# Kernel optimization log

Measured on AMD Instinct MI355X. Metric: run time of the kernel, lower is better.

Reference implementation:

```python
import jax, jax.numpy as jnp
import numpy as np

B, N, C, H, T = 64, 4096, 768, 12, 10


def setup_inputs() -> dict:
    key = jax.random.key(0)
    kx, kq, kk, kv, kp = jax.random.split(key, 5)
    std = 0.02  # trunc_normal std from _init_weights
    return {
        "x": jax.random.normal(kx, (B, N, C), jnp.float32),
        "Wq": std * jax.random.normal(kq, (C, C), jnp.float32),
        "Wk": std * jax.random.normal(kk, (C, C), jnp.float32),
        "Wv": std * jax.random.normal(kv, (C, C), jnp.float32),
        "Wp": std * jax.random.normal(kp, (C, C), jnp.float32),
        "bp": jnp.zeros((C,), jnp.float32),
        "nb_task_tokens": T,
    }


def reference(x, Wq, Wk, Wv, Wp, bp, nb_task_tokens):
    Bq, Nq, Cq = x.shape
    d = Cq // H
    scale = d ** -0.5
    Tt = nb_task_tokens
    # q only from the first T (task) tokens; k, v from all N tokens
    q = (x[:, :Tt] @ Wq).reshape(Bq, Tt, H, d).transpose(0, 2, 1, 3) * scale  # [B,H,T,d]
    k = (x @ Wk).reshape(Bq, Nq, H, d).transpose(0, 2, 1, 3)                  # [B,H,N,d]
    v = (x @ Wv).reshape(Bq, Nq, H, d).transpose(0, 2, 1, 3)                  # [B,H,N,d]
    attn = jnp.einsum("bhtd,bhnd->bhtn", q, k)                                # [B,H,T,N]
    # mask: task token i may attend to itself and to all patch tokens (cols >= T),
    # but not to other task tokens
    rows = jnp.arange(Tt)[:, None]
    cols = jnp.arange(Nq)[None, :]
    allowed = (cols >= Tt) | (cols == rows)                                   # [T,N]
    attn = jnp.where(allowed, attn, -jnp.inf)
    attn = jax.nn.softmax(attn, axis=-1)
    x_cls = jnp.einsum("bhtn,bhnd->bhtd", attn, v)                            # [B,H,T,d]
    x_cls = x_cls.transpose(0, 2, 1, 3).reshape(Bq, Tt, Cq)
    x_cls = x_cls @ Wp + bp
    return (x_cls, attn, v)
```

## Files before the change

kernel.cpp:

```cpp
#include <hip/hip_runtime.h>

typedef __attribute__((ext_vector_type(8))) short short8;
typedef __attribute__((ext_vector_type(4))) short short4v;
typedef __attribute__((ext_vector_type(4))) float f32x4;

__device__ __forceinline__ unsigned short f2bf(float f) {
  union { float f; unsigned u; } v; v.f = f;
  unsigned r = v.u + 0x7FFFu + ((v.u >> 16) & 1u);
  return (unsigned short)(r >> 16);
}

__device__ __forceinline__ float bf2f(unsigned short h) {
  union { unsigned u; float f; } v; v.u = ((unsigned)h) << 16;
  return v.f;
}

__device__ __forceinline__ void gload16(const void* g, void* l) {
  __builtin_amdgcn_global_load_lds(
      (const __attribute__((address_space(1))) void*)g,
      (__attribute__((address_space(3))) void*)l, 16, 0, 0);
}

__global__ __launch_bounds__(256) void conv_x(const float* __restrict__ x,
                                              unsigned short* __restrict__ xb) {
  const long total = 25165824;
  long stride = (long)gridDim.x * 256;
  for (long u = blockIdx.x * 256 + threadIdx.x; u < total; u += stride) {
    const float* p = x + u * 8;
    float4 a = *(const float4*)p;
    float4 b = *(const float4*)(p + 4);
    short8 h;
    h[0] = (short)f2bf(a.x); h[1] = (short)f2bf(a.y);
    h[2] = (short)f2bf(a.z); h[3] = (short)f2bf(a.w);
    h[4] = (short)f2bf(b.x); h[5] = (short)f2bf(b.y);
    h[6] = (short)f2bf(b.z); h[7] = (short)f2bf(b.w);
    *(short8*)(xb + u * 8) = h;
  }
}

__global__ __launch_bounds__(256) void prep_w(const float* __restrict__ Wk,
                                              const float* __restrict__ Wv,
                                              unsigned short* __restrict__ Wt) {
  int idx = blockIdx.x * 256 + threadIdx.x;
  int n = idx / 768, k = idx - n * 768;
  float w = (n < 768) ? Wk[k * 768 + n] : Wv[k * 768 + (n - 768)];
  Wt[idx] = f2bf(w);
}

__global__ __launch_bounds__(256) void q_proj(const float* __restrict__ x,
                                              const float* __restrict__ Wq,
                                              unsigned short* __restrict__ q_ws) {
  int b = blockIdx.x, tid = threadIdx.x;
  __shared__ float xr[7680];
  const float* xp = x + (long)b * 4096 * 768;
  for (int i = tid; i < 7680; i += 256) xr[i] = xp[i];
  for (int i = tid; i < 12 * 6 * 64; i += 256) {
    int h = i / 384, rem = i - h * 384;
    int t = 10 + rem / 64, d = rem & 63;
    q_ws[(((long)(b * 12 + h) * 16 + t) << 6) + d] = 0;
  }
  __syncthreads();
  float acc[10][3];
#pragma unroll
  for (int t = 0; t < 10; ++t) { acc[t][0] = 0.f; acc[t][1] = 0.f; acc[t][2] = 0.f; }
  for (int k = 0; k < 768; ++k) {
    const float* wr = Wq + (long)k * 768;
    float w0 = wr[tid], w1 = wr[tid + 256], w2 = wr[tid + 512];
#pragma unroll
    for (int t = 0; t < 10; ++t) {
      float xv = xr[t * 768 + k];
      acc[t][0] += xv * w0; acc[t][1] += xv * w1; acc[t][2] += xv * w2;
    }
  }
#pragma unroll
  for (int t = 0; t < 10; ++t) {
#pragma unroll
    for (int j = 0; j < 3; ++j) {
      int c = tid + j * 256;
      int h = c >> 6, d = c & 63;
      q_ws[(((long)(b * 12 + h) * 16 + t) << 6) + d] = f2bf(acc[t][j] * 0.125f);
    }
  }
}

#define SGA(AT, I, KO) gload16(sA + (long)(I) * 49152 + (KO), (AT) + ((I) * 64 + uw * 8) * 64)
#define SGB(BT, I, KO) gload16(sB + (long)(I) * 49152 + (KO), (BT) + ((I) * 64 + uw * 8) * 64)
#define WBND asm volatile("s_waitcnt vmcnt(0)\n\ts_barrier" ::: "memory")
#define PBAR __builtin_amdgcn_s_barrier()

#define BODY(AC, BC, AN, BN, KOS, DOST)                                         \
  {                                                                             \
    short8 fa[4][2], fb0[2][2], fb1[2][2];                                      \
    if (DOST) { SGA(AN, 0, KOS); SGA(AN, 1, KOS); SGB(BN, 0, KOS); SGB(BN, 1, KOS); } \
    _Pragma("unroll")                                                           \
    for (int mi = 0; mi < 4; ++mi) {                                            \
      fa[mi][0] = *(const short8*)&AC[arb + mi * 1024 + ck0];                   \
      fa[mi][1] = *(const short8*)&AC[arb + mi * 1024 + ck1];                   \
    }                                                                           \
    _Pragma("unroll")                                                           \
    for (int ni = 0; ni < 2; ++ni) {                                            \
      fb0[ni][0] = *(const short8*)&BC[brb + ni * 1024 + ck0];                  \
      fb0[ni][1] = *(const short8*)&BC[brb + ni * 1024 + ck1];                  \
    }                                                                           \
    PBAR;                                                                       \
    __builtin_amdgcn_s_setprio(1);                                              \
    _Pragma("unroll")                                                           \
    for (int mi = 0; mi < 4; ++mi)                                              \
      _Pragma("unroll")                                                         \
      for (int ni = 0; ni < 2; ++ni) {                                          \
        acc[mi][ni] = __builtin_amdgcn_mfma_f32_16x16x32_bf16(fa[mi][0], fb0[ni][0], acc[mi][ni], 0, 0, 0); \
        acc[mi][ni] = __builtin_amdgcn_mfma_f32_16x16x32_bf16(fa[mi][1], fb0[ni][1], acc[mi][ni], 0, 0, 0); \
      }                                                                         \
    __builtin_amdgcn_s_setprio(0);                                              \
    PBAR;                                                                       \
    if (DOST) { SGA(AN, 2, KOS); SGA(AN, 3, KOS); SGB(BN, 2, KOS); SGB(BN, 3, KOS); } \
    _Pragma("unroll")                                                           \
    for (int ni = 0; ni < 2; ++ni) {                                            \
      fb1[ni][0] = *(const short8*)&BC[brb + (ni + 2) * 1024 + ck0];            \
      fb1[ni][1] = *(const short8*)&BC[brb + (ni + 2) * 1024 + ck1];            \
    }                                                                           \
    PBAR;                                                                       \
    __builtin_amdgcn_s_setprio(1);                                              \
    _Pragma("unroll")                                                           \
    for (int mi = 0; mi < 4; ++mi)                                              \
      _Pragma("unroll")                                                         \
      for (int ni = 0; ni < 2; ++ni) {                                          \
        acc[mi][ni + 2] = __builtin_amdgcn_mfma_f32_16x16x32_bf16(fa[mi][0], fb1[ni][0], acc[mi][ni + 2], 0, 0, 0); \
        acc[mi][ni + 2] = __builtin_amdgcn_mfma_f32_16x16x32_bf16(fa[mi][1], fb1[ni][1], acc[mi][ni + 2], 0, 0, 0); \
      }                                                                         \
    __builtin_amdgcn_s_setprio(0);                                              \
    PBAR;                                                                       \
    _Pragma("unroll")                                                           \
    for (int mi = 0; mi < 4; ++mi) {                                            \
      fa[mi][0] = *(const short8*)&AC[arb + (mi + 4) * 1024 + ck0];             \
      fa[mi][1] = *(const short8*)&AC[arb + (mi + 4) * 1024 + ck1];             \
    }                                                                           \
    PBAR;                                                                       \
    __builtin_amdgcn_s_setprio(1);                                              \
    _Pragma("unroll")                                                           \
    for (int mi = 0; mi < 4; ++mi)                                              \
      _Pragma("unroll")                                                         \
      for (int ni = 0; ni < 2; ++ni) {                                          \
        acc[mi + 4][ni + 2] = __builtin_amdgcn_mfma_f32_16x16x32_bf16(fa[mi][0], fb1[ni][0], acc[mi + 4][ni + 2], 0, 0, 0); \
        acc[mi + 4][ni + 2] = __builtin_amdgcn_mfma_f32_16x16x32_bf16(fa[mi][1], fb1[ni][1], acc[mi + 4][ni + 2], 0, 0, 0); \
      }                                                                         \
    __builtin_amdgcn_s_setprio(0);                                              \
    PBAR;                                                                       \
    __builtin_amdgcn_s_setprio(1);                                              \
    _Pragma("unroll")                                                           \
    for (int mi = 0; mi < 4; ++mi)                                              \
      _Pragma("unroll")                                                         \
      for (int ni = 0; ni < 2; ++ni) {                                          \
        acc[mi + 4][ni] = __builtin_amdgcn_mfma_f32_16x16x32_bf16(fa[mi][0], fb0[ni][0], acc[mi + 4][ni], 0, 0, 0); \
        acc[mi + 4][ni] = __builtin_amdgcn_mfma_f32_16x16x32_bf16(fa[mi][1], fb0[ni][1], acc[mi + 4][ni], 0, 0, 0); \
      }                                                                         \
    __builtin_amdgcn_s_setprio(0);                                              \
  }

#define GEMM_PROLOGUE                                                           \
  int bid = blockIdx.x;                                                         \
  int lb = (bid & 7) * 768 + (bid >> 3);                                        \
  int mt = lb / 6;                                                              \
  int nt = lb - mt * 6;                                                         \
  long m0 = (long)mt * 256;                                                     \
  int n0 = nt * 256;                                                            \
  int tid = threadIdx.x;                                                        \
  int lane = tid & 63;                                                          \
  int uw = __builtin_amdgcn_readfirstlane(tid >> 6);                            \
  int wm = uw >> 2;                                                             \
  int wn = uw & 3;                                                              \
  int r16 = lane & 15;                                                          \
  int gk = lane >> 4;                                                           \
  const unsigned short* xs = xb + m0 * 768;                                     \
  const unsigned short* wp = Wt + (long)n0 * 768;                               \
  int srow8 = lane >> 3;                                                        \
  int sch = ((lane & 7) ^ (srow8 & 7)) << 3;                                    \
  const unsigned short* sA = xs + (long)(uw * 8 + srow8) * 768 + sch;           \
  const unsigned short* sB = wp + (long)(uw * 8 + srow8) * 768 + sch;           \
  int ck0 = ((gk ^ (r16 & 7)) << 3);                                            \
  int ck1 = (((4 + gk) ^ (r16 & 7)) << 3);                                      \
  int arb = (wm * 128 + r16) * 64;                                              \
  int brb = (wn * 64 + r16) * 64;                                               \
  f32x4 acc[8][4];                                                              \
  _Pragma("unroll")                                                             \
  for (int i = 0; i < 8; ++i)                                                   \
    _Pragma("unroll")                                                           \
    for (int j = 0; j < 4; ++j) acc[i][j] = (f32x4){0.f, 0.f, 0.f, 0.f};        \
  SGA(A0T, 0, 0); SGA(A0T, 1, 0); SGA(A0T, 2, 0); SGA(A0T, 3, 0);               \
  SGB(B0T, 0, 0); SGB(B0T, 1, 0); SGB(B0T, 2, 0); SGB(B0T, 3, 0);               \
  WBND;                                                                         \
  _Pragma("unroll 1")                                                           \
  for (int t = 0; t < 12; t += 2) {                                             \
    BODY(A0T, B0T, A1T, B1T, (t + 1) * 64, true);                               \
    WBND;                                                                       \
    BODY(A1T, B1T, A0T, B0T, (t + 2) * 64, (t + 2) < 12);                       \
    WBND;                                                                       \
  }

__global__ __launch_bounds__(512, 2) void gemm_kv9(const unsigned short* __restrict__ xb,
                                                   const unsigned short* __restrict__ Wt,
                                                   unsigned short* __restrict__ k_ws,
                                                   float* __restrict__ v_out,
                                                   unsigned short* __restrict__ vt) {
  __shared__ char smem[131072];
  unsigned short* A0T = (unsigned short*)(smem);
  unsigned short* B0T = (unsigned short*)(smem + 32768);
  unsigned short* A1T = (unsigned short*)(smem + 65536);
  unsigned short* B1T = (unsigned short*)(smem + 98304);
  GEMM_PROLOGUE

  float* scr0 = (float*)smem + uw * 2176;
  float* scr1 = scr0 + 1088;
  bool is_k = (n0 < 768);
  int h = (is_k ? (n0 >> 6) : ((n0 - 768) >> 6)) + wn;
  int bq = (int)(m0 >> 12);
  int nb = (int)(m0 & 4095) + wm * 128;

  if (is_k) {
#pragma unroll
    for (int mi = 0; mi < 8; ++mi) {
#pragma unroll
      for (int ni = 0; ni < 4; ++ni)
#pragma unroll
        for (int r = 0; r < 4; ++r)
          scr0[(gk * 4 + r) * 68 + ni * 16 + r16] = acc[mi][ni][r];
      int nbase = nb + mi * 16;
#pragma unroll
      for (int p = 0; p < 2; ++p) {
        int row = p * 8 + (lane >> 3);
        int d0 = (lane & 7) << 3;
        float4 aa = *(const float4*)&scr0[row * 68 + d0];
        float4 bb = *(const float4*)&scr0[row * 68 + d0 + 4];
        short8 hh;
        hh[0] = (short)f2bf(aa.x); hh[1] = (short)f2bf(aa.y);
        hh[2] = (short)f2bf(aa.z); hh[3] = (short)f2bf(aa.w);
        hh[4] = (short)f2bf(bb.x); hh[5] = (short)f2bf(bb.y);
        hh[6] = (short)f2bf(bb.z); hh[7] = (short)f2bf(bb.w);
        *(short8*)&k_ws[((long)(bq * 12 + h) * 4096 + nbase + row) * 64 + d0] = hh;
      }
    }
  } else {
    unsigned short* vTp = vt + ((long)(bq * 12 + h) * 64) * 4096;
#pragma unroll
    for (int mp = 0; mp < 4; ++mp) {
      int nbase = nb + mp * 32;
#pragma unroll
      for (int ni = 0; ni < 4; ++ni)
#pragma unroll
        for (int r = 0; r < 4; ++r) {
          scr0[(gk * 4 + r) * 68 + ni * 16 + r16] = acc[mp * 2][ni][r];
          scr1[(gk * 4 + r) * 68 + ni * 16 + r16] = acc[mp * 2 + 1][ni][r];
        }
#pragma unroll
      for (int p = 0; p < 4; ++p) {
        int row = p * 4 + (lane >> 4);
        int d0 = (lane & 15) << 2;
        float4 a0 = *(const float4*)&scr0[row * 68 + d0];
        *(float4*)&v_out[((long)(bq * 12 + h) * 4096 + nbase + row) * 64 + d0] = a0;
        float4 a1 = *(const float4*)&scr1[row * 68 + d0];
        *(float4*)&v_out[((long)(bq * 12 + h) * 4096 + nbase + 16 + row) * 64 + d0] = a1;
      }
      short8 w0;
      short8 w1;
      short8 w2;
      short8 w3;
#pragma unroll
      for (int i = 0; i < 8; ++i) {
        w0[i] = (short)f2bf(scr0[i * 68 + lane]);
        w1[i] = (short)f2bf(scr0[(i + 8) * 68 + lane]);
        w2[i] = (short)f2bf(scr1[i * 68 + lane]);
        w3[i] = (short)f2bf(scr1[(i + 8) * 68 + lane]);
      }
      unsigned short* vrow = vTp + (long)lane * 4096 + nbase;
      *(short8*)(vrow)      = w0;
      *(short8*)(vrow + 8)  = w1;
      *(short8*)(vrow + 16) = w2;
      *(short8*)(vrow + 24) = w3;
    }
  }
}

__global__ __launch_bounds__(512, 2) void gemm_kv8(const unsigned short* __restrict__ xb,
                                                   const unsigned short* __restrict__ Wt,
                                                   unsigned short* __restrict__ k_ws,
                                                   float* __restrict__ v_out) {
  __shared__ char smem[131072];
  unsigned short* A0T = (unsigned short*)(smem);
  unsigned short* B0T = (unsigned short*)(smem + 32768);
  unsigned short* A1T = (unsigned short*)(smem + 65536);
  unsigned short* B1T = (unsigned short*)(smem + 98304);
  GEMM_PROLOGUE

  float* scr = (float*)smem + uw * 1088;
  bool is_k = (n0 < 768);
  int h = (is_k ? (n0 >> 6) : ((n0 - 768) >> 6)) + wn;
  int bq = (int)(m0 >> 12);
  int nb = (int)(m0 & 4095) + wm * 128;
#pragma unroll
  for (int mi = 0; mi < 8; ++mi) {
#pragma unroll
    for (int ni = 0; ni < 4; ++ni)
#pragma unroll
      for (int r = 0; r < 4; ++r)
        scr[(gk * 4 + r) * 68 + ni * 16 + r16] = acc[mi][ni][r];
    int nbase = nb + mi * 16;
    if (is_k) {
#pragma unroll
      for (int p = 0; p < 2; ++p) {
        int row = p * 8 + (lane >> 3);
        int d0 = (lane & 7) << 3;
        float4 aa = *(const float4*)&scr[row * 68 + d0];
        float4 bb = *(const float4*)&scr[row * 68 + d0 + 4];
        short8 hh;
        hh[0] = (short)f2bf(aa.x); hh[1] = (short)f2bf(aa.y);
        hh[2] = (short)f2bf(aa.z); hh[3] = (short)f2bf(aa.w);
        hh[4] = (short)f2bf(bb.x); hh[5] = (short)f2bf(bb.y);
        hh[6] = (short)f2bf(bb.z); hh[7] = (short)f2bf(bb.w);
        *(short8*)&k_ws[((long)(bq * 12 + h) * 4096 + nbase + row) * 64 + d0] = hh;
      }
    } else {
#pragma unroll
      for (int p = 0; p < 4; ++p) {
        int row = p * 4 + (lane >> 4);
        int d0 = (lane & 15) << 2;
        float4 aa = *(const float4*)&scr[row * 68 + d0];
        *(float4*)&v_out[((long)(bq * 12 + h) * 4096 + nbase + row) * 64 + d0] = aa;
      }
    }
  }
}

#undef GEMM_PROLOGUE
#undef BODY
#undef SGA
#undef SGB
#undef WBND
#undef PBAR

__global__ __launch_bounds__(256) void gemm_kv(const float* __restrict__ x,
                                               const unsigned short* __restrict__ Wt,
                                               unsigned short* __restrict__ k_ws,
                                               float* __restrict__ v_out) {
  __shared__ char lds[32768];
  int bid = blockIdx.x;
  int lb = (bid & 7) * 3072 + (bid >> 3);
  int mt = lb / 12, nt = lb - mt * 12;
  long m0 = (long)mt * 128; int n0 = nt * 128;
  int tid = threadIdx.x, lane = tid & 63;
  int wid = tid >> 6, wm = wid >> 1, wn = wid & 1;
  int rlo = lane & 15, gk = lane >> 4;

  const float* xs = x + m0 * 768;
  const unsigned short* wp = Wt + (long)n0 * 768;

  int arow0 = tid >> 3, ak4 = (tid & 7) << 2;
  int bn = tid >> 1, bg = (tid & 1) << 1;

  f32x4 acc[4][4];
#pragma unroll
  for (int i = 0; i < 4; ++i)
#pragma unroll
    for (int j = 0; j < 4; ++j) acc[i][j] = (f32x4){0.f, 0.f, 0.f, 0.f};

  float4 fA[4]; short8 wB[2];
#pragma unroll
  for (int it = 0; it < 4; ++it) {
    int row = it * 32 + arow0;
    fA[it] = *(const float4*)(xs + (long)row * 768 + ak4);
  }
#pragma unroll
  for (int i = 0; i < 2; ++i)
    wB[i] = *(const short8*)(wp + (long)bn * 768 + (bg + i) * 8);
#pragma unroll
  for (int it = 0; it < 4; ++it) {
    int row = it * 32 + arow0;
    short4v h;
    h[0] = (short)f2bf(fA[it].x); h[1] = (short)f2bf(fA[it].y);
    h[2] = (short)f2bf(fA[it].z); h[3] = (short)f2bf(fA[it].w);
    *(short4v*)(lds + row * 64 + ((ak4 * 2) ^ (((row >> 1) & 3) << 4))) = h;
  }
#pragma unroll
  for (int i = 0; i < 2; ++i)
    *(short8*)(lds + 16384 + bn * 64 + (((bg + i) * 16) ^ (((bn >> 1) & 3) << 4))) = wB[i];
  __syncthreads();

#pragma unroll 2
  for (int ks = 0; ks < 24; ++ks) {
    char* Ab = lds + (ks & 1) * 8192;
    char* Bb = lds + 16384 + (ks & 1) * 8192;
    bool pf = (ks + 1 < 24);
    if (pf) {
#pragma unroll
      for (int it = 0; it < 4; ++it) {
        int row = it * 32 + arow0;
        fA[it] = *(const float4*)(xs + (long)row * 768 + (ks + 1) * 32 + ak4);
      }
#pragma unroll
      for (int i = 0; i < 2; ++i)
        wB[i] = *(const short8*)(wp + (long)bn * 768 + (ks + 1) * 32 + (bg + i) * 8);
    }
    short8 af[4], bfr[4];
#pragma unroll
    for (int mi = 0; mi < 4; ++mi) {
      int row = wm * 64 + mi * 16 + rlo;
      af[mi] = *(const short8*)(Ab + row * 64 + ((gk * 16) ^ (((row >> 1) & 3) << 4)));
    }
#pragma unroll
    for (int ni = 0; ni < 4; ++ni) {
      int n = wn * 64 + ni * 16 + rlo;
      bfr[ni] = *(const short8*)(Bb + n * 64 + ((gk * 16) ^ (((n >> 1) & 3) << 4)));
    }
#pragma unroll
    for (int mi = 0; mi < 4; ++mi)
#pragma unroll
      for (int ni = 0; ni < 4; ++ni)
        acc[mi][ni] = __builtin_amdgcn_mfma_f32_16x16x32_bf16(af[mi], bfr[ni], acc[mi][ni], 0, 0, 0);
    if (pf) {
      char* An = lds + ((ks + 1) & 1) * 8192;
      char* Bn = lds + 16384 + ((ks + 1) & 1) * 8192;
#pragma unroll
      for (int it = 0; it < 4; ++it) {
        int row = it * 32 + arow0;
        short4v h;
        h[0] = (short)f2bf(fA[it].x); h[1] = (short)f2bf(fA[it].y);
        h[2] = (short)f2bf(fA[it].z); h[3] = (short)f2bf(fA[it].w);
        *(short4v*)(An + row * 64 + ((ak4 * 2) ^ (((row >> 1) & 3) << 4))) = h;
      }
#pragma unroll
      for (int i = 0; i < 2; ++i)
        *(short8*)(Bn + bn * 64 + (((bg + i) * 16) ^ (((bn >> 1) & 3) << 4))) = wB[i];
    }
    __syncthreads();
  }

  bool is_k = (n0 < 768);
  int cb = is_k ? n0 : n0 - 768;
#pragma unroll
  for (int ni = 0; ni < 4; ++ni) {
    int cc = cb + wn * 64 + ni * 16 + rlo;
    int h = cc >> 6, d = cc & 63;
#pragma unroll
    for (int mi = 0; mi < 4; ++mi) {
#pragma unroll
      for (int r = 0; r < 4; ++r) {
        long m = m0 + wm * 64 + mi * 16 + gk * 4 + r;
        int b = (int)(m >> 12), n = (int)(m & 4095);
        long off = ((long)(b * 12 + h) * 4096 + n) * 64 + d;
        float val = acc[mi][ni][r];
        if (is_k) k_ws[off] = f2bf(val);
        else      v_out[off] = val;
      }
    }
  }
}

__global__ __launch_bounds__(512) void attn_fused4(const unsigned short* __restrict__ k_ws,
                                                   const unsigned short* __restrict__ q_ws,
                                                   const unsigned short* __restrict__ vt,
                                                   float* __restrict__ attn_out,
                                                   float* __restrict__ preproj) {
  __shared__ char blob[115712];
  unsigned short* pbuf = (unsigned short*)blob;
  float* part = (float*)(blob + 81920);
  float* redm = (float*)(blob + 114688);
  float* rowmax16 = redm + 128;
  float* rowinv16 = rowmax16 + 16;

  int tid = threadIdx.x, lane = tid & 63, w = tid >> 6;
  int bh = blockIdx.x;
  int r16 = lane & 15, gk = lane >> 4;
  int trc = (r16 < 10) ? r16 : 9;
  int nW = w << 9;

  const unsigned short* kp = k_ws + (long)bh * (4096 * 64);
  const unsigned short* qp = q_ws + (long)bh * 1024;
  float* sraw = attn_out + (long)bh * 40960;
  const unsigned short* vtp = vt + (long)bh * (64 * 4096);

  short8 qf0 = *(const short8*)(qp + r16 * 64 + gk * 8);
  short8 qf1 = *(const short8*)(qp + r16 * 64 + 32 + gk * 8);

  char* pbw = (char*)pbuf + w * 10240 + r16 * 1024;
  int swz = (r16 & 7) << 4;

  float pmax = -3.0e38f;
#pragma unroll 4
  for (int ch = 0; ch < 32; ++ch) {
    int n0 = nW + (ch << 4);
    short8 kf0 = *(const short8*)(kp + (long)(n0 + r16) * 64 + gk * 8);
    short8 kf1 = *(const short8*)(kp + (long)(n0 + r16) * 64 + 32 + gk * 8);
    f32x4 d4 = (f32x4){0.f, 0.f, 0.f, 0.f};
    d4 = __builtin_amdgcn_mfma_f32_16x16x32_bf16(kf0, qf0, d4, 0, 0, 0);
    d4 = __builtin_amdgcn_mfma_f32_16x16x32_bf16(kf1, qf1, d4, 0, 0, 0);
#pragma unroll
    for (int r = 0; r < 4; ++r) {
      int n = n0 + gk * 4 + r;
      float v = d4[r];
      if (n < 10 && n != r16) v = -1e30f;
      d4[r] = v;
      pmax = fmaxf(pmax, v);
    }
    if (r16 < 10) {
      short4v h4;
      h4[0] = (short)f2bf(d4[0]); h4[1] = (short)f2bf(d4[1]);
      h4[2] = (short)f2bf(d4[2]); h4[3] = (short)f2bf(d4[3]);
      *(short4v*)(pbw + ((ch * 32 + gk * 8) ^ swz)) = h4;
    }
  }
  pmax = fmaxf(pmax, __shfl_xor(pmax, 16));
  pmax = fmaxf(pmax, __shfl_xor(pmax, 32));
  if (lane < 16) redm[w * 16 + lane] = pmax;
  __syncthreads();
  if (tid < 16) {
    float m = redm[tid];
#pragma unroll
    for (int i = 1; i < 8; ++i) m = fmaxf(m, redm[i * 16 + tid]);
    rowmax16[tid] = m;
  }
  __syncthreads();

  float mx = rowmax16[trc];
  char* pbr = (char*)pbuf + w * 10240 + trc * 1024;
  int swr = (trc & 7) << 4;
  float psum = 0.f;
#pragma unroll 4
  for (int i = 0; i < 16; ++i) {
    short8 sv = *(const short8*)(pbr + ((i * 64 + gk * 16) ^ swr));
#pragma unroll
    for (int j = 0; j < 8; ++j) psum += __expf(bf2f((unsigned short)sv[j]) - mx);
  }
  psum += __shfl_xor(psum, 16);
  psum += __shfl_xor(psum, 32);
  if (lane < 16) redm[w * 16 + lane] = psum;
  __syncthreads();
  if (tid < 16) {
    float t = 0.f;
#pragma unroll
    for (int i = 0; i < 8; ++i) t += redm[i * 16 + tid];
    rowinv16[tid] = 1.0f / t;
  }
  __syncthreads();
  float inv = rowinv16[trc];

  if (r16 < 10) {
#pragma unroll 4
    for (int i = 0; i < 16; ++i) {
      short8 sv = *(const short8*)(pbw + ((i * 64 + gk * 16) ^ swz));
      float4 o0, o1;
      o0.x = __expf(bf2f((unsigned short)sv[0]) - mx) * inv;
      o0.y = __expf(bf2f((unsigned short)sv[1]) - mx) * inv;
      o0.z = __expf(bf2f((unsigned short)sv[2]) - mx) * inv;
      o0.w = __expf(bf2f((unsigned short)sv[3]) - mx) * inv;
      o1.x = __expf(bf2f((unsigned short)sv[4]) - mx) * inv;
      o1.y = __expf(bf2f((unsigned short)sv[5]) - mx) * inv;
      o1.z = __expf(bf2f((unsigned short)sv[6]) - mx) * inv;
      o1.w = __expf(bf2f((unsigned short)sv[7]) - mx) * inv;
      float* gp = sraw + r16 * 4096 + nW + i * 32 + gk * 8;
      *(float4*)gp = o0;
      *(float4*)(gp + 4) = o1;
    }
  }

  f32x4 pacc[4];
#pragma unroll
  for (int dc = 0; dc < 4; ++dc) pacc[dc] = (f32x4){0.f, 0.f, 0.f, 0.f};
#pragma unroll 2
  for (int ks = 0; ks < 16; ++ks) {
    short8 raw = *(const short8*)(pbr + ((ks * 64 + gk * 16) ^ swr));
    short8 pa;
#pragma unroll
    for (int j = 0; j < 8; ++j)
      pa[j] = (short)f2bf(__expf(bf2f((unsigned short)raw[j]) - mx) * inv);
    int nbb = nW + ks * 32 + gk * 8;
#pragma unroll
    for (int dc = 0; dc < 4; ++dc) {
      short8 vb = *(const short8*)&vtp[(long)(dc * 16 + r16) * 4096 + nbb];
      pacc[dc] = __builtin_amdgcn_mfma_f32_16x16x32_bf16(pa, vb, pacc[dc], 0, 0, 0);
    }
  }
#pragma unroll
  for (int dc = 0; dc < 4; ++dc)
#pragma unroll
    for (int r = 0; r < 4; ++r)
      part[w * 1024 + dc * 256 + (gk * 4 + r) * 16 + r16] = pacc[dc][r];
  __syncthreads();

  int b = bh / 12, h = bh - b * 12;
  for (int idx = tid; idx < 640; idx += 512) {
    int tt = idx >> 6, d = idx & 63;
    int dc = d >> 4, dl = d & 15;
    float sum = 0.f;
#pragma unroll
    for (int i = 0; i < 8; ++i) sum += part[i * 1024 + dc * 256 + tt * 16 + dl];
    preproj[((long)b * 10 + tt) * 768 + h * 64 + d] = sum;
  }
}

__global__ __launch_bounds__(512) void attn_fused3(const unsigned short* __restrict__ k_ws,
                                                   const unsigned short* __restrict__ q_ws,
                                                   const float* __restrict__ v_glob,
                                                   float* __restrict__ attn_out,
                                                   float* __restrict__ preproj) {
  __shared__ char blob[115712];
  unsigned short* pbuf = (unsigned short*)blob;
  float* part = (float*)(blob + 81920);
  float* redm = (float*)(blob + 114688);
  float* rowmax16 = redm + 128;
  float* rowinv16 = rowmax16 + 16;

  int tid = threadIdx.x, lane = tid & 63, w = tid >> 6;
  int bh = blockIdx.x;
  int r16 = lane & 15, gk = lane >> 4;
  int trc = (r16 < 10) ? r16 : 9;
  int nW = w << 9;

  const unsigned short* kp = k_ws + (long)bh * (4096 * 64);
  const unsigned short* qp = q_ws + (long)bh * 1024;
  float* sraw = attn_out + (long)bh * 40960;
  const float* vp = v_glob + (long)bh * (4096 * 64);

  short8 qf0 = *(const short8*)(qp + r16 * 64 + gk * 8);
  short8 qf1 = *(const short8*)(qp + r16 * 64 + 32 + gk * 8);

  char* pbw = (char*)pbuf + w * 10240 + r16 * 1024;
  int swz = (r16 & 7) << 4;

  float pmax = -3.0e38f;
#pragma unroll 4
  for (int ch = 0; ch < 32; ++ch) {
    int n0 = nW + (ch << 4);
    short8 kf0 = *(const short8*)(kp + (long)(n0 + r16) * 64 + gk * 8);
    short8 kf1 = *(const short8*)(kp + (long)(n0 + r16) * 64 + 32 + gk * 8);
    f32x4 d4 = (f32x4){0.f, 0.f, 0.f, 0.f};
    d4 = __builtin_amdgcn_mfma_f32_16x16x32_bf16(kf0, qf0, d4, 0, 0, 0);
    d4 = __builtin_amdgcn_mfma_f32_16x16x32_bf16(kf1, qf1, d4, 0, 0, 0);
#pragma unroll
    for (int r = 0; r < 4; ++r) {
      int n = n0 + gk * 4 + r;
      float v = d4[r];
      if (n < 10 && n != r16) v = -1e30f;
      d4[r] = v;
      pmax = fmaxf(pmax, v);
    }
    if (r16 < 10) {
      short4v h4;
      h4[0] = (short)f2bf(d4[0]); h4[1] = (short)f2bf(d4[1]);
      h4[2] = (short)f2bf(d4[2]); h4[3] = (short)f2bf(d4[3]);
      *(short4v*)(pbw + ((ch * 32 + gk * 8) ^ swz)) = h4;
    }
  }
  pmax = fmaxf(pmax, __shfl_xor(pmax, 16));
  pmax = fmaxf(pmax, __shfl_xor(pmax, 32));
  if (lane < 16) redm[w * 16 + lane] = pmax;
  __syncthreads();
  if (tid < 16) {
    float m = redm[tid];
#pragma unroll
    for (int i = 1; i < 8; ++i) m = fmaxf(m, redm[i * 16 + tid]);
    rowmax16[tid] = m;
  }
  __syncthreads();

  float mx = rowmax16[trc];
  char* pbr = (char*)pbuf + w * 10240 + trc * 1024;
  int swr = (trc & 7) << 4;
  float psum = 0.f;
#pragma unroll 4
  for (int i = 0; i < 16; ++i) {
    short8 sv = *(const short8*)(pbr + ((i * 64 + gk * 16) ^ swr));
#pragma unroll
    for (int j = 0; j < 8; ++j) psum += __expf(bf2f((unsigned short)sv[j]) - mx);
  }
  psum += __shfl_xor(psum, 16);
  psum += __shfl_xor(psum, 32);
  if (lane < 16) redm[w * 16 + lane] = psum;
  __syncthreads();
  if (tid < 16) {
    float t = 0.f;
#pragma unroll
    for (int i = 0; i < 8; ++i) t += redm[i * 16 + tid];
    rowinv16[tid] = 1.0f / t;
  }
  __syncthreads();
  float inv = rowinv16[trc];

  if (r16 < 10) {
#pragma unroll 4
    for (int i = 0; i < 16; ++i) {
      short8 sv = *(const short8*)(pbw + ((i * 64 + gk * 16) ^ swz));
      float4 o0, o1;
      o0.x = __expf(bf2f((unsigned short)sv[0]) - mx) * inv;
      o0.y = __expf(bf2f((unsigned short)sv[1]) - mx) * inv;
      o0.z = __expf(bf2f((unsigned short)sv[2]) - mx) * inv;
      o0.w = __expf(bf2f((unsigned short)sv[3]) - mx) * inv;
      o1.x = __expf(bf2f((unsigned short)sv[4]) - mx) * inv;
      o1.y = __expf(bf2f((unsigned short)sv[5]) - mx) * inv;
      o1.z = __expf(bf2f((unsigned short)sv[6]) - mx) * inv;
      o1.w = __expf(bf2f((unsigned short)sv[7]) - mx) * inv;
      float* gp = sraw + r16 * 4096 + nW + i * 32 + gk * 8;
      *(float4*)gp = o0;
      *(float4*)(gp + 4) = o1;
    }
  }

  f32x4 pacc[4];
#pragma unroll
  for (int dc = 0; dc < 4; ++dc) pacc[dc] = (f32x4){0.f, 0.f, 0.f, 0.f};
#pragma unroll 2
  for (int ks = 0; ks < 16; ++ks) {
    short8 raw = *(const short8*)(pbr + ((ks * 64 + gk * 16) ^ swr));
    short8 pa;
#pragma unroll
    for (int j = 0; j < 8; ++j)
      pa[j] = (short)f2bf(__expf(bf2f((unsigned short)raw[j]) - mx) * inv);
    const float* vbase = vp + (long)(nW + ks * 32 + gk * 8) * 64 + r16;
#pragma unroll
    for (int dc = 0; dc < 4; ++dc) {
      short8 vb;
      const float* vrow = vbase + dc * 16;
#pragma unroll
      for (int j = 0; j < 8; ++j) vb[j] = (short)f2bf(vrow[j * 64]);
      pacc[dc] = __builtin_amdgcn_mfma_f32_16x16x32_bf16(pa, vb, pacc[dc], 0, 0, 0);
    }
  }
#pragma unroll
  for (int dc = 0; dc < 4; ++dc)
#pragma unroll
    for (int r = 0; r < 4; ++r)
      part[w * 1024 + dc * 256 + (gk * 4 + r) * 16 + r16] = pacc[dc][r];
  __syncthreads();

  int b = bh / 12, h = bh - b * 12;
  for (int idx = tid; idx < 640; idx += 512) {
    int tt = idx >> 6, d = idx & 63;
    int dc = d >> 4, dl = d & 15;
    float sum = 0.f;
#pragma unroll
    for (int i = 0; i < 8; ++i) sum += part[i * 1024 + dc * 256 + tt * 16 + dl];
    preproj[((long)b * 10 + tt) * 768 + h * 64 + d] = sum;
  }
}

__global__ __launch_bounds__(256) void proj_out_k(const float* __restrict__ preproj,
                                                  const float* __restrict__ Wp,
                                                  const float* __restrict__ bp,
                                                  float* __restrict__ out0) {
  int b = blockIdx.x, tid = threadIdx.x;
  __shared__ float xr[7680];
  const float* pp = preproj + (long)b * 7680;
  for (int i = tid; i < 7680; i += 256) xr[i] = pp[i];
  __syncthreads();
  float acc[10][3];
#pragma unroll
  for (int t = 0; t < 10; ++t) { acc[t][0] = 0.f; acc[t][1] = 0.f; acc[t][2] = 0.f; }
  for (int k = 0; k < 768; ++k) {
    const float* wr = Wp + (long)k * 768;
    float w0 = wr[tid], w1 = wr[tid + 256], w2 = wr[tid + 512];
#pragma unroll
    for (int t = 0; t < 10; ++t) {
      float xv = xr[t * 768 + k];
      acc[t][0] += xv * w0; acc[t][1] += xv * w1; acc[t][2] += xv * w2;
    }
  }
  float b0 = bp[tid], b1 = bp[tid + 256], b2 = bp[tid + 512];
  float* op = out0 + (long)b * 7680;
#pragma unroll
  for (int t = 0; t < 10; ++t) {
    op[t * 768 + tid]       = acc[t][0] + b0;
    op[t * 768 + tid + 256] = acc[t][1] + b1;
    op[t * 768 + tid + 512] = acc[t][2] + b2;
  }
}

extern "C" void kernel_launch(void* const* d_in, const int* in_sizes, int n_in,
                              void* d_out, int out_size, void* d_ws, size_t ws_size,
                              hipStream_t stream) {
  (void)in_sizes; (void)n_in; (void)out_size;
  const float* x  = (const float*)d_in[0];
  const float* Wq = (const float*)d_in[1];
  const float* Wk = (const float*)d_in[2];
  const float* Wv = (const float*)d_in[3];
  const float* Wp = (const float*)d_in[4];
  const float* bp = (const float*)d_in[5];

  float* out      = (float*)d_out;
  float* attn_out = out + 491520;
  float* v_out    = out + 31948800;

  char* ws = (char*)d_ws;
  const size_t NEED_VT  = 1213857792;
  const size_t NEED_BIG = 811204608;

  if (ws_size >= NEED_VT) {
    unsigned short* x_bf16 = (unsigned short*)(ws);
    unsigned short* k_ws   = (unsigned short*)(ws + 402653184);
    unsigned short* vt_ws  = (unsigned short*)(ws + 805306368);
    unsigned short* q_ws   = (unsigned short*)(ws + 1207959552);
    unsigned short* Wt     = (unsigned short*)(ws + 1209532416);
    float* preproj         = (float*)(ws + 1211891712);

    conv_x<<<dim3(2048), dim3(256), 0, stream>>>(x, x_bf16);
    prep_w<<<dim3(4608), dim3(256), 0, stream>>>(Wk, Wv, Wt);
    q_proj<<<dim3(64), dim3(256), 0, stream>>>(x, Wq, q_ws);
    gemm_kv9<<<dim3(6144), dim3(512), 0, stream>>>(x_bf16, Wt, k_ws, v_out, vt_ws);
    attn_fused4<<<dim3(768), dim3(512), 0, stream>>>(k_ws, q_ws, vt_ws, attn_out, preproj);
    proj_out_k<<<dim3(64), dim3(256), 0, stream>>>(preproj, Wp, bp, out);
  } else if (ws_size >= NEED_BIG) {
    unsigned short* x_bf16 = (unsigned short*)(ws);
    unsigned short* k_ws   = (unsigned short*)(ws + 402653184);
    unsigned short* q_ws   = (unsigned short*)(ws + 805306368);
    unsigned short* Wt     = (unsigned short*)(ws + 806879232);
    float* preproj         = (float*)(ws + 809238528);

    conv_x<<<dim3(2048), dim3(256), 0, stream>>>(x, x_bf16);
    prep_w<<<dim3(4608), dim3(256), 0, stream>>>(Wk, Wv, Wt);
    q_proj<<<dim3(64), dim3(256), 0, stream>>>(x, Wq, q_ws);
    gemm_kv8<<<dim3(6144), dim3(512), 0, stream>>>(x_bf16, Wt, k_ws, v_out);
    attn_fused3<<<dim3(768), dim3(512), 0, stream>>>(k_ws, q_ws, v_out, attn_out, preproj);
    proj_out_k<<<dim3(64), dim3(256), 0, stream>>>(preproj, Wp, bp, out);
  } else {
    unsigned short* k_ws = (unsigned short*)(ws);
    unsigned short* q_ws = (unsigned short*)(ws + 402653184);
    unsigned short* Wt   = (unsigned short*)(ws + 404226048);
    float* preproj       = (float*)(ws + 406585344);

    prep_w<<<dim3(4608), dim3(256), 0, stream>>>(Wk, Wv, Wt);
    q_proj<<<dim3(64), dim3(256), 0, stream>>>(x, Wq, q_ws);
    gemm_kv<<<dim3(24576), dim3(256), 0, stream>>>(x, Wt, k_ws, v_out);
    attn_fused3<<<dim3(768), dim3(512), 0, stream>>>(k_ws, q_ws, v_out, attn_out, preproj);
    proj_out_k<<<dim3(64), dim3(256), 0, stream>>>(preproj, Wp, bp, out);
  }
}
```

Baseline: 1.567 ms.

## Fuse fp32-to-bf16 conversion of x into the KV GEMM A-tile load

Removes the separate conv_x pass and its bf16 copy of x. The GEMM now loads fp32 x into registers, converts to bf16 and writes swizzled LDS tiles between MFMA phases, instead of using direct global-to-LDS loads. The V-transpose epilogue now writes bf16 directly from the accumulators rather than staging through a second scratch buffer. This saves a full read and write of the 400MB bf16 intermediate, at the cost of twice the A-side global traffic inside the GEMM plus more registers and VALU work in the main loop. The workspace need shrinks, so the vt path now runs at the smaller workspace threshold.

```diff
diff --git a/kernel.cpp b/kernel.cpp
--- a/kernel.cpp
+++ b/kernel.cpp
@@ -19,23 +19,6 @@
   __builtin_amdgcn_global_load_lds(
       (const __attribute__((address_space(1))) void*)g,
       (__attribute__((address_space(3))) void*)l, 16, 0, 0);
-}
-
-__global__ __launch_bounds__(256) void conv_x(const float* __restrict__ x,
-                                              unsigned short* __restrict__ xb) {
-  const long total = 25165824;
-  long stride = (long)gridDim.x * 256;
-  for (long u = blockIdx.x * 256 + threadIdx.x; u < total; u += stride) {
-    const float* p = x + u * 8;
-    float4 a = *(const float4*)p;
-    float4 b = *(const float4*)(p + 4);
-    short8 h;
-    h[0] = (short)f2bf(a.x); h[1] = (short)f2bf(a.y);
-    h[2] = (short)f2bf(a.z); h[3] = (short)f2bf(a.w);
-    h[4] = (short)f2bf(b.x); h[5] = (short)f2bf(b.y);
-    h[6] = (short)f2bf(b.z); h[7] = (short)f2bf(b.w);
-    *(short8*)(xb + u * 8) = h;
-  }
 }
 
 __global__ __launch_bounds__(256) void prep_w(const float* __restrict__ Wk,
@@ -83,15 +66,30 @@
   }
 }
 
-#define SGA(AT, I, KO) gload16(sA + (long)(I) * 49152 + (KO), (AT) + ((I) * 64 + uw * 8) * 64)
 #define SGB(BT, I, KO) gload16(sB + (long)(I) * 49152 + (KO), (BT) + ((I) * 64 + uw * 8) * 64)
-#define WBND asm volatile("s_waitcnt vmcnt(0)\n\ts_barrier" ::: "memory")
+#define WBND2 asm volatile("s_waitcnt vmcnt(0) lgkmcnt(0)\n\ts_barrier" ::: "memory")
 #define PBAR __builtin_amdgcn_s_barrier()
+
+#define ALOAD(KO)                                                               \
+  _Pragma("unroll")                                                             \
+  for (int i = 0; i < 8; ++i)                                                   \
+    ax[i] = *(const float4*)(pAx + i * 3072 + (KO));
+
+#define AWRITE(AN, I0)                                                          \
+  _Pragma("unroll")                                                             \
+  for (int i = I0; i < I0 + 4; ++i) {                                           \
+    int row = rowc + i * 4;                                                     \
+    short4v h4;                                                                 \
+    h4[0] = (short)f2bf(ax[i].x); h4[1] = (short)f2bf(ax[i].y);                 \
+    h4[2] = (short)f2bf(ax[i].z); h4[3] = (short)f2bf(ax[i].w);                 \
+    *(short4v*)((char*)(AN) + row * 128 +                                       \
+                ((((kq >> 1) ^ (row & 7)) << 4) | ((kq & 1) << 3))) = h4;       \
+  }
 
 #define BODY(AC, BC, AN, BN, KOS, DOST)                                         \
   {                                                                             \
     short8 fa[4][2], fb0[2][2], fb1[2][2];                                      \
-    if (DOST) { SGA(AN, 0, KOS); SGA(AN, 1, KOS); SGB(BN, 0, KOS); SGB(BN, 1, KOS); } \
+    if (DOST) { ALOAD(KOS); SGB(BN, 0, KOS); SGB(BN, 1, KOS); }                 \
     _Pragma("unroll")                                                           \
     for (int mi = 0; mi < 4; ++mi) {                                            \
       fa[mi][0] = *(const short8*)&AC[arb + mi * 1024 + ck0];                   \
@@ -113,7 +111,7 @@
       }                                                                         \
     __builtin_amdgcn_s_setprio(0);                                              \
     PBAR;                                                                       \
-    if (DOST) { SGA(AN, 2, KOS); SGA(AN, 3, KOS); SGB(BN, 2, KOS); SGB(BN, 3, KOS); } \
+    if (DOST) { SGB(BN, 2, KOS); SGB(BN, 3, KOS); }                             \
     _Pragma("unroll")                                                           \
     for (int ni = 0; ni < 2; ++ni) {                                            \
       fb1[ni][0] = *(const short8*)&BC[brb + (ni + 2) * 1024 + ck0];            \
@@ -130,6 +128,7 @@
       }                                                                         \
     __builtin_amdgcn_s_setprio(0);                                              \
     PBAR;                                                                       \
+    if (DOST) { AWRITE(AN, 0); }                                                \
     _Pragma("unroll")                                                           \
     for (int mi = 0; mi < 4; ++mi) {                                            \
       fa[mi][0] = *(const short8*)&AC[arb + (mi + 4) * 1024 + ck0];             \
@@ -146,6 +145,7 @@
       }                                                                         \
     __builtin_amdgcn_s_setprio(0);                                              \
     PBAR;                                                                       \
+    if (DOST) { AWRITE(AN, 4); }                                                \
     __builtin_amdgcn_s_setprio(1);                                              \
     _Pragma("unroll")                                                           \
     for (int mi = 0; mi < 4; ++mi)                                              \
@@ -157,154 +157,83 @@
     __builtin_amdgcn_s_setprio(0);                                              \
   }
 
-#define GEMM_PROLOGUE                                                           \
-  int bid = blockIdx.x;                                                         \
-  int lb = (bid & 7) * 768 + (bid >> 3);                                        \
-  int mt = lb / 6;                                                              \
-  int nt = lb - mt * 6;                                                         \
-  long m0 = (long)mt * 256;                                                     \
-  int n0 = nt * 256;                                                            \
-  int tid = threadIdx.x;                                                        \
-  int lane = tid & 63;                                                          \
-  int uw = __builtin_amdgcn_readfirstlane(tid >> 6);                            \
-  int wm = uw >> 2;                                                             \
-  int wn = uw & 3;                                                              \
-  int r16 = lane & 15;                                                          \
-  int gk = lane >> 4;                                                           \
-  const unsigned short* xs = xb + m0 * 768;                                     \
-  const unsigned short* wp = Wt + (long)n0 * 768;                               \
-  int srow8 = lane >> 3;                                                        \
-  int sch = ((lane & 7) ^ (srow8 & 7)) << 3;                                    \
-  const unsigned short* sA = xs + (long)(uw * 8 + srow8) * 768 + sch;           \
-  const unsigned short* sB = wp + (long)(uw * 8 + srow8) * 768 + sch;           \
-  int ck0 = ((gk ^ (r16 & 7)) << 3);                                            \
-  int ck1 = (((4 + gk) ^ (r16 & 7)) << 3);                                      \
-  int arb = (wm * 128 + r16) * 64;                                              \
-  int brb = (wn * 64 + r16) * 64;                                               \
-  f32x4 acc[8][4];                                                              \
-  _Pragma("unroll")                                                             \
-  for (int i = 0; i < 8; ++i)                                                   \
-    _Pragma("unroll")                                                           \
-    for (int j = 0; j < 4; ++j) acc[i][j] = (f32x4){0.f, 0.f, 0.f, 0.f};        \
-  SGA(A0T, 0, 0); SGA(A0T, 1, 0); SGA(A0T, 2, 0); SGA(A0T, 3, 0);               \
-  SGB(B0T, 0, 0); SGB(B0T, 1, 0); SGB(B0T, 2, 0); SGB(B0T, 3, 0);               \
-  WBND;                                                                         \
-  _Pragma("unroll 1")                                                           \
-  for (int t = 0; t < 12; t += 2) {                                             \
-    BODY(A0T, B0T, A1T, B1T, (t + 1) * 64, true);                               \
-    WBND;                                                                       \
-    BODY(A1T, B1T, A0T, B0T, (t + 2) * 64, (t + 2) < 12);                       \
-    WBND;                                                                       \
-  }
-
-__global__ __launch_bounds__(512, 2) void gemm_kv9(const unsigned short* __restrict__ xb,
-                                                   const unsigned short* __restrict__ Wt,
-                                                   unsigned short* __restrict__ k_ws,
-                                                   float* __restrict__ v_out,
-                                                   unsigned short* __restrict__ vt) {
+__global__ __launch_bounds__(512, 2) void gemm_kv10(const float* __restrict__ x,
+                                                    const unsigned short* __restrict__ Wt,
+                                                    unsigned short* __restrict__ k_ws,
+                                                    float* __restrict__ v_out,
+                                                    unsigned short* __restrict__ vt) {
   __shared__ char smem[131072];
   unsigned short* A0T = (unsigned short*)(smem);
   unsigned short* B0T = (unsigned short*)(smem + 32768);
   unsigned short* A1T = (unsigned short*)(smem + 65536);
   unsigned short* B1T = (unsigned short*)(smem + 98304);
-  GEMM_PROLOGUE
-
-  float* scr0 = (float*)smem + uw * 2176;
-  float* scr1 = scr0 + 1088;
-  bool is_k = (n0 < 768);
-  int h = (is_k ? (n0 >> 6) : ((n0 - 768) >> 6)) + wn;
-  int bq = (int)(m0 >> 12);
-  int nb = (int)(m0 & 4095) + wm * 128;
-
-  if (is_k) {
-#pragma unroll
-    for (int mi = 0; mi < 8; ++mi) {
-#pragma unroll
-      for (int ni = 0; ni < 4; ++ni)
-#pragma unroll
-        for (int r = 0; r < 4; ++r)
-          scr0[(gk * 4 + r) * 68 + ni * 16 + r16] = acc[mi][ni][r];
-      int nbase = nb + mi * 16;
-#pragma unroll
-      for (int p = 0; p < 2; ++p) {
-        int row = p * 8 + (lane >> 3);
-        int d0 = (lane & 7) << 3;
-        float4 aa = *(const float4*)&scr0[row * 68 + d0];
-        float4 bb = *(const float4*)&scr0[row * 68 + d0 + 4];
-        short8 hh;
-        hh[0] = (short)f2bf(aa.x); hh[1] = (short)f2bf(aa.y);
-        hh[2] = (short)f2bf(aa.z); hh[3] = (short)f2bf(aa.w);
-        hh[4] = (short)f2bf(bb.x); hh[5] = (short)f2bf(bb.y);
-        hh[6] = (short)f2bf(bb.z); hh[7] = (short)f2bf(bb.w);
-        *(short8*)&k_ws[((long)(bq * 12 + h) * 4096 + nbase + row) * 64 + d0] = hh;
-      }
-    }
-  } else {
-    unsigned short* vTp = vt + ((long)(bq * 12 + h) * 64) * 4096;
-#pragma unroll
-    for (int mp = 0; mp < 4; ++mp) {
-      int nbase = nb + mp * 32;
-#pragma unroll
-      for (int ni = 0; ni < 4; ++ni)
-#pragma unroll
-        for (int r = 0; r < 4; ++r) {
-          scr0[(gk * 4 + r) * 68 + ni * 16 + r16] = acc[mp * 2][ni][r];
-          scr1[(gk * 4 + r) * 68 + ni * 16 + r16] = acc[mp * 2 + 1][ni][r];
-        }
-#pragma unroll
-      for (int p = 0; p < 4; ++p) {
-        int row = p * 4 + (lane >> 4);
-        int d0 = (lane & 15) << 2;
-        float4 a0 = *(const float4*)&scr0[row * 68 + d0];
-        *(float4*)&v_out[((long)(bq * 12 + h) * 4096 + nbase + row) * 64 + d0] = a0;
-        float4 a1 = *(const float4*)&scr1[row * 68 + d0];
-        *(float4*)&v_out[((long)(bq * 12 + h) * 4096 + nbase + 16 + row) * 64 + d0] = a1;
-      }
-      short8 w0;
-      short8 w1;
-      short8 w2;
-      short8 w3;
-#pragma unroll
-      for (int i = 0; i < 8; ++i) {
-        w0[i] = (short)f2bf(scr0[i * 68 + lane]);
-        w1[i] = (short)f2bf(scr0[(i + 8) * 68 + lane]);
-        w2[i] = (short)f2bf(scr1[i * 68 + lane]);
-        w3[i] = (short)f2bf(scr1[(i + 8) * 68 + lane]);
-      }
-      unsigned short* vrow = vTp + (long)lane * 4096 + nbase;
-      *(short8*)(vrow)      = w0;
-      *(short8*)(vrow + 8)  = w1;
-      *(short8*)(vrow + 16) = w2;
-      *(short8*)(vrow + 24) = w3;
-    }
-  }
-}
-
-__global__ __launch_bounds__(512, 2) void gemm_kv8(const unsigned short* __restrict__ xb,
-                                                   const unsigned short* __restrict__ Wt,
-                                                   unsigned short* __restrict__ k_ws,
-                                                   float* __restrict__ v_out) {
-  __shared__ char smem[131072];
-  unsigned short* A0T = (unsigned short*)(smem);
-  unsigned short* B0T = (unsigned short*)(smem + 32768);
-  unsigned short* A1T = (unsigned short*)(smem + 65536);
-  unsigned short* B1T = (unsigned short*)(smem + 98304);
-  GEMM_PROLOGUE
+
+  int bid = blockIdx.x;
+  int lb = (bid & 7) * 768 + (bid >> 3);
+  int mt = lb / 6;
+  int nt = lb - mt * 6;
+  long m0 = (long)mt * 256;
+  int n0 = nt * 256;
+  int tid = threadIdx.x;
+  int lane = tid & 63;
+  int uw = __builtin_amdgcn_readfirstlane(tid >> 6);
+  int wm = uw >> 2;
+  int wn = uw & 3;
+  int r16 = lane & 15;
+  int gk = lane >> 4;
+
+  const unsigned short* wp = Wt + (long)n0 * 768;
+
+  int rowL = lane >> 4;
+  int kq = lane & 15;
+  int rowc = uw * 32 + rowL;
+  const float* pAx = x + (m0 + rowc) * 768 + kq * 4;
+
+  int srow8 = lane >> 3;
+  int sch = ((lane & 7) ^ (srow8 & 7)) << 3;
+  const unsigned short* sB = wp + (long)(uw * 8 + srow8) * 768 + sch;
+
+  int ck0 = ((gk ^ (r16 & 7)) << 3);
+  int ck1 = (((4 + gk) ^ (r16 & 7)) << 3);
+  int arb = (wm * 128 + r16) * 64;
+  int brb = (wn * 64 + r16) * 64;
+
+  float4 ax[8];
+  f32x4 acc[8][4];
+#pragma unroll
+  for (int i = 0; i < 8; ++i)
+#pragma unroll
+    for (int j = 0; j < 4; ++j) acc[i][j] = (f32x4){0.f, 0.f, 0.f, 0.f};
+
+  ALOAD(0);
+  SGB(B0T, 0, 0); SGB(B0T, 1, 0); SGB(B0T, 2, 0); SGB(B0T, 3, 0);
+  AWRITE(A0T, 0);
+  AWRITE(A0T, 4);
+  WBND2;
+
+#pragma unroll 1
+  for (int t = 0; t < 12; t += 2) {
+    BODY(A0T, B0T, A1T, B1T, (t + 1) * 64, true);
+    WBND2;
+    BODY(A1T, B1T, A0T, B0T, (t + 2) * 64, (t + 2) < 12);
+    WBND2;
+  }
 
   float* scr = (float*)smem + uw * 1088;
   bool is_k = (n0 < 768);
   int h = (is_k ? (n0 >> 6) : ((n0 - 768) >> 6)) + wn;
   int bq = (int)(m0 >> 12);
   int nb = (int)(m0 & 4095) + wm * 128;
-#pragma unroll
-  for (int mi = 0; mi < 8; ++mi) {
-#pragma unroll
-    for (int ni = 0; ni < 4; ++ni)
-#pragma unroll
-      for (int r = 0; r < 4; ++r)
-        scr[(gk * 4 + r) * 68 + ni * 16 + r16] = acc[mi][ni][r];
-    int nbase = nb + mi * 16;
-    if (is_k) {
+
+  if (is_k) {
+#pragma unroll
+    for (int mi = 0; mi < 8; ++mi) {
+#pragma unroll
+      for (int ni = 0; ni < 4; ++ni)
+#pragma unroll
+        for (int r = 0; r < 4; ++r)
+          scr[(gk * 4 + r) * 68 + ni * 16 + r16] = acc[mi][ni][r];
+      int nbase = nb + mi * 16;
 #pragma unroll
       for (int p = 0; p < 2; ++p) {
         int row = p * 8 + (lane >> 3);
@@ -318,7 +247,17 @@
         hh[6] = (short)f2bf(bb.z); hh[7] = (short)f2bf(bb.w);
         *(short8*)&k_ws[((long)(bq * 12 + h) * 4096 + nbase + row) * 64 + d0] = hh;
       }
-    } else {
+    }
+  } else {
+    unsigned short* vTp = vt + (long)(bq * 12 + h) * 64 * 4096;
+#pragma unroll
+    for (int mi = 0; mi < 8; ++mi) {
+#pragma unroll
+      for (int ni = 0; ni < 4; ++ni)
+#pragma unroll
+        for (int r = 0; r < 4; ++r)
+          scr[(gk * 4 + r) * 68 + ni * 16 + r16] = acc[mi][ni][r];
+      int nbase = nb + mi * 16;
 #pragma unroll
       for (int p = 0; p < 4; ++p) {
         int row = p * 4 + (lane >> 4);
@@ -326,15 +265,24 @@
         float4 aa = *(const float4*)&scr[row * 68 + d0];
         *(float4*)&v_out[((long)(bq * 12 + h) * 4096 + nbase + row) * 64 + d0] = aa;
       }
-    }
-  }
-}
-
-#undef GEMM_PROLOGUE
+#pragma unroll
+      for (int ni = 0; ni < 4; ++ni) {
+        short4v h4;
+        h4[0] = (short)f2bf(acc[mi][ni][0]);
+        h4[1] = (short)f2bf(acc[mi][ni][1]);
+        h4[2] = (short)f2bf(acc[mi][ni][2]);
+        h4[3] = (short)f2bf(acc[mi][ni][3]);
+        *(short4v*)&vTp[(long)(ni * 16 + r16) * 4096 + nbase + gk * 4] = h4;
+      }
+    }
+  }
+}
+
 #undef BODY
-#undef SGA
+#undef ALOAD
+#undef AWRITE
 #undef SGB
-#undef WBND
+#undef WBND2
 #undef PBAR
 
 __global__ __launch_bounds__(256) void gemm_kv(const float* __restrict__ x,
@@ -788,35 +736,19 @@
   float* v_out    = out + 31948800;
 
   char* ws = (char*)d_ws;
-  const size_t NEED_VT  = 1213857792;
-  const size_t NEED_BIG = 811204608;
-
-  if (ws_size >= NEED_VT) {
-    unsigned short* x_bf16 = (unsigned short*)(ws);
-    unsigned short* k_ws   = (unsigned short*)(ws + 402653184);
-    unsigned short* vt_ws  = (unsigned short*)(ws + 805306368);
-    unsigned short* q_ws   = (unsigned short*)(ws + 1207959552);
-    unsigned short* Wt     = (unsigned short*)(ws + 1209532416);
-    float* preproj         = (float*)(ws + 1211891712);
-
-    conv_x<<<dim3(2048), dim3(256), 0, stream>>>(x, x_bf16);
+  const size_t NEED = 811204608;
+
+  if (ws_size >= NEED) {
+    unsigned short* k_ws  = (unsigned short*)(ws);
+    unsigned short* vt_ws = (unsigned short*)(ws + 402653184);
+    unsigned short* q_ws  = (unsigned short*)(ws + 805306368);
+    unsigned short* Wt    = (unsigned short*)(ws + 806879232);
+    float* preproj        = (float*)(ws + 809238528);
+
     prep_w<<<dim3(4608), dim3(256), 0, stream>>>(Wk, Wv, Wt);
     q_proj<<<dim3(64), dim3(256), 0, stream>>>(x, Wq, q_ws);
-    gemm_kv9<<<dim3(6144), dim3(512), 0, stream>>>(x_bf16, Wt, k_ws, v_out, vt_ws);
+    gemm_kv10<<<dim3(6144), dim3(512), 0, stream>>>(x, Wt, k_ws, v_out, vt_ws);
     attn_fused4<<<dim3(768), dim3(512), 0, stream>>>(k_ws, q_ws, vt_ws, attn_out, preproj);
-    proj_out_k<<<dim3(64), dim3(256), 0, stream>>>(preproj, Wp, bp, out);
-  } else if (ws_size >= NEED_BIG) {
-    unsigned short* x_bf16 = (unsigned short*)(ws);
-    unsigned short* k_ws   = (unsigned short*)(ws + 402653184);
-    unsigned short* q_ws   = (unsigned short*)(ws + 805306368);
-    unsigned short* Wt     = (unsigned short*)(ws + 806879232);
-    float* preproj         = (float*)(ws + 809238528);
-
-    conv_x<<<dim3(2048), dim3(256), 0, stream>>>(x, x_bf16);
-    prep_w<<<dim3(4608), dim3(256), 0, stream>>>(Wk, Wv, Wt);
-    q_proj<<<dim3(64), dim3(256), 0, stream>>>(x, Wq, q_ws);
-    gemm_kv8<<<dim3(6144), dim3(512), 0, stream>>>(x_bf16, Wt, k_ws, v_out);
-    attn_fused3<<<dim3(768), dim3(512), 0, stream>>>(k_ws, q_ws, v_out, attn_out, preproj);
     proj_out_k<<<dim3(64), dim3(256), 0, stream>>>(preproj, Wp, bp, out);
   } else {
     unsigned short* k_ws = (unsigned short*)(ws);
```

Measured after the change: 1.651 ms. 1.05x slower.
